# Performance work log

Measured on AMD Instinct MI355X. Metric: run time of the kernel, lower is better.

Reference implementation:

```python
import jax, jax.numpy as jnp
import numpy as np

B, N, K = 8, 2048, 20
IN_CHAN = 3
CONV_DIMS = (64, 64, 128, 256)
FEAT_DIM = 1024
SLOPE = 0.2  # LeakyReLU negative slope (DGCNN standard)


def setup_inputs() -> dict:
    key = jax.random.key(0)
    ks = jax.random.split(key, 11)
    x = jax.random.normal(ks[0], (B, N, IN_CHAN), dtype=jnp.float32)
    in_dims = (IN_CHAN,) + CONV_DIMS[:-1]
    inp = {"x": x}
    for i, (cin, cout) in enumerate(zip(in_dims, CONV_DIMS)):
        inp[f"W{i+1}"] = jax.random.normal(ks[1 + 2 * i], (cout, 2 * cin), dtype=jnp.float32) * 0.05
        inp[f"b{i+1}"] = jnp.zeros((cout,), dtype=jnp.float32)
    inp["Wf"] = jax.random.normal(ks[9], (FEAT_DIM, sum(CONV_DIMS)), dtype=jnp.float32) * 0.05
    inp["bf"] = jnp.zeros((FEAT_DIM,), dtype=jnp.float32)
    return inp


def _knn_idx(x, k):
    # x: (B, N, C) -> indices of k nearest neighbors (self included), (B, N, K)
    xx = jnp.sum(x * x, axis=-1)                       # (B, N)
    inner = jnp.einsum('bnc,bmc->bnm', x, x)           # (B, N, N)
    d2 = xx[:, :, None] - 2.0 * inner + xx[:, None, :]  # squared distances
    _, idx = jax.lax.top_k(-d2, k)                     # k smallest distances
    return idx


def _edge_conv(x, W, b, k):
    # x: (B, N, C); W: (O, 2C); b: (O,) -> (B, N, O)
    idx = _knn_idx(x, k)                               # (B, N, K)
    nbr = jax.vmap(lambda xb, ib: xb[ib])(x, idx)      # (B, N, K, C) gather
    center = jnp.broadcast_to(x[:, :, None, :], nbr.shape)
    feat = jnp.concatenate([nbr - center, center], axis=-1)  # (B, N, K, 2C)
    h = jnp.einsum('bnkc,oc->bnko', feat, W) + b       # 1x1 conv over edges
    h = jax.nn.leaky_relu(h, SLOPE)
    return jnp.max(h, axis=2)                          # max over neighbors


def reference(x, W1, b1, W2, b2, W3, b3, W4, b4, Wf, bf):
    params = [(W1, b1), (W2, b2), (W3, b3), (W4, b4)]
    feats = []
    h = x
    for W, b in params:
        h = _edge_conv(h, W, b, K)
        feats.append(h)
    hcat = jnp.concatenate(feats, axis=-1)             # (B, N, sum(conv_dims))
    out = jnp.einsum('bnc,oc->bno', hcat, Wf) + bf     # final 1x1 conv
    out = jax.nn.leaky_relu(out, SLOPE)
    return jnp.max(out, axis=1)                        # global max pool -> (B, FEAT_DIM)
```

## Files before the change

### kernel.cpp

```cpp
#include <hip/hip_runtime.h>

constexpr int B_ = 8;
constexpr int N_ = 2048;
constexpr int K_ = 20;
constexpr float SLOPE_ = 0.2f;

typedef __attribute__((ext_vector_type(8))) short bf16x8;
typedef __attribute__((ext_vector_type(8))) _Float16 f16x8;
typedef __attribute__((ext_vector_type(4))) float f32x4;

__device__ __forceinline__ float lrelu(float v) { return v > 0.0f ? v : SLOPE_ * v; }

__device__ __forceinline__ void async16(const void* g, void* l) {
  __builtin_amdgcn_global_load_lds((const __attribute__((address_space(1))) unsigned int*)g,
                                   (__attribute__((address_space(3))) unsigned int*)l, 16, 0, 0);
}

__device__ __forceinline__ unsigned long long shflx64(unsigned long long v, int m) {
  return __shfl_xor(v, m, 64);
}

__device__ __forceinline__ unsigned short f2bf(float f) {
  unsigned u = __float_as_uint(f);
  u += 0x7fff + ((u >> 16) & 1);
  return (unsigned short)(u >> 16);
}

__device__ __forceinline__ unsigned short f2h(float f) {
  _Float16 h = (_Float16)f;
  return __builtin_bit_cast(unsigned short, h);
}
__device__ __forceinline__ float h2f(unsigned short u) {
  return (float)__builtin_bit_cast(_Float16, u);
}

__global__ void prep_wp(const float* __restrict__ W, float* __restrict__ Wp, int O, int C) {
  int i = blockIdx.x * 256 + threadIdx.x;
  if (i >= 2 * O * C) return;
  int o = i / C, c = i - o * C;
  if (o < O)
    Wp[i] = W[o * 2 * C + c];
  else
    Wp[i] = W[(o - O) * 2 * C + C + c] - W[(o - O) * 2 * C + c];
}

__global__ void cvt_bf16(const float4* __restrict__ src, ushort4* __restrict__ dst, int n4) {
  int i = blockIdx.x * 256 + threadIdx.x;
  if (i >= n4) return;
  float4 v = src[i];
  ushort4 o = {f2bf(v.x), f2bf(v.y), f2bf(v.z), f2bf(v.w)};
  dst[i] = o;
}

__global__ void norms_x(const float* __restrict__ x, float* __restrict__ xx) {
  int i = blockIdx.x * 256 + threadIdx.x;
  if (i >= B_ * N_) return;
  const float* p = x + (size_t)i * 3;
  xx[i] = p[0] * p[0] + p[1] * p[1] + p[2] * p[2];
}

__global__ void split32_x(const float* __restrict__ x, unsigned short* __restrict__ xh,
                          unsigned short* __restrict__ xm) {
  int id = blockIdx.x * 256 + threadIdx.x;
  if (id >= B_ * N_ * 32) return;
  int row = id >> 5, c = id & 31;
  float val = (c < 3) ? x[row * 3 + c] : 0.0f;
  unsigned short hb = f2h(val);
  float vh = h2f(hb);
  xh[id] = hb;
  xm[id] = f2h(val - vh);
}

template <int C>
__global__ void pack_knn(const unsigned short* __restrict__ Xh,
                         const unsigned short* __restrict__ Xm,
                         unsigned short* __restrict__ Pk) {
  constexpr int KK = C / 32;
  int id = blockIdx.x * 256 + threadIdx.x;
  const int outoff = id;
  const int l = id & 63;
  id >>= 6;
  const int split = id & 1;
  id >>= 1;
  const int kk = id % KK;
  id /= KK;
  const int tile = id & 127;
  const int b = id >> 7;
  const unsigned short* src = (split == 0) ? Xh : Xm;
  const size_t soff =
      (size_t)(b * N_ + tile * 16 + (l & 15)) * C + (size_t)kk * 32 + (size_t)(l >> 4) * 8;
  uint4 v = *(const uint4*)(src + soff);
  *(uint4*)(Pk + (size_t)outoff * 8) = v;
}

template <int C>
__global__ __launch_bounds__(1024, 4) void knn_mfma(const unsigned short* __restrict__ Pk,
                                                    const unsigned short* __restrict__ Xh,
                                                    const unsigned short* __restrict__ Xm,
                                                    const float* __restrict__ xx,
                                                    int* __restrict__ idxo) {
  constexpr int KK = C / 32;
  constexpr int DP = 3;
  constexpr int NIT = KK * 8;
  const int b = blockIdx.x & 7;
  const int q0 = (blockIdx.x >> 3) * 16;
  const int tid = threadIdx.x;
  const int w = tid >> 6, lane = tid & 63;
  const int bN = b * N_;
  const int lr = lane & 15;
  const int lk = (lane >> 4) * 8;

  __shared__ float d2s[16][2052];
  __shared__ unsigned long long cbuf[16][64];

  const size_t qoff = (size_t)(bN + q0 + lr) * C + lk;
  f16x8 a2h[2], a2m[2];
  a2h[0] = *(const f16x8*)(Xh + qoff);
  a2m[0] = *(const f16x8*)(Xm + qoff);

  f32x4 acc[8];
#pragma unroll
  for (int t = 0; t < 8; t++) acc[t] = (f32x4){0.0f, 0.0f, 0.0f, 0.0f};

  const size_t pbase = (size_t)b * (128 * KK * 2 * 512) + (size_t)lane * 8;
  f16x8 bh[DP], bm[DP];
#pragma unroll
  for (int i = 0; i < DP; i++) {
    const size_t a = pbase + (size_t)(((w * 8 + i) * KK + 0) * 2) * 512;
    bh[i] = *(const f16x8*)(Pk + a);
    bm[i] = *(const f16x8*)(Pk + a + 512);
  }
#pragma unroll
  for (int it = 0; it < NIT; it++) {
    const int kk = it >> 3, t = it & 7, s = it % DP;
    if (t == 0 && kk + 1 < KK) {
      const size_t qa = qoff + (size_t)(kk + 1) * 32;
      a2h[(kk + 1) & 1] = *(const f16x8*)(Xh + qa);
      a2m[(kk + 1) & 1] = *(const f16x8*)(Xm + qa);
    }
    f16x8 vh = bh[s], vm = bm[s];
    if (it + DP < NIT) {
      const int it2 = it + DP;
      const int kk2 = it2 >> 3, t2 = it2 & 7;
      const size_t a = pbase + (size_t)(((w * 8 + t2) * KK + kk2) * 2) * 512;
      bh[s] = *(const f16x8*)(Pk + a);
      bm[s] = *(const f16x8*)(Pk + a + 512);
    }
    const f16x8 ah = a2h[kk & 1], am = a2m[kk & 1];
    acc[t] = __builtin_amdgcn_mfma_f32_16x16x32_f16(ah, vh, acc[t], 0, 0, 0);
    acc[t] = __builtin_amdgcn_mfma_f32_16x16x32_f16(ah, vm, acc[t], 0, 0, 0);
    acc[t] = __builtin_amdgcn_mfma_f32_16x16x32_f16(am, vh, acc[t], 0, 0, 0);
    acc[t] = __builtin_amdgcn_mfma_f32_16x16x32_f16(am, vm, acc[t], 0, 0, 0);
  }

  float qn[4];
#pragma unroll
  for (int r = 0; r < 4; r++) qn[r] = xx[bN + q0 + (lane >> 4) * 4 + r];
#pragma unroll
  for (int t = 0; t < 8; t++) {
    float cn = xx[bN + (w * 8 + t) * 16 + lr];
#pragma unroll
    for (int r = 0; r < 4; r++) {
      float v = fmaxf(fmaf(-2.0f, acc[t][r], cn + qn[r]), 0.0f);
      d2s[(lane >> 4) * 4 + r][(w * 8 + t) * 16 + lr] = v;
    }
  }
  __syncthreads();

  float r2[32];
#pragma unroll
  for (int i = 0; i < 32; i++) r2[i] = d2s[w][i * 64 + lane];

  const float INF = __int_as_float(0x7f800000);
  unsigned long long* cb = cbuf[w];
  int* outp = idxo + (size_t)(bN + q0 + w) * K_;

  float lmin = r2[0];
#pragma unroll
  for (int i = 1; i < 32; i++) lmin = fminf(lmin, r2[i]);
  float sv = lmin;
#pragma unroll
  for (int k = 2; k <= 64; k <<= 1)
#pragma unroll
    for (int j = k >> 1; j > 0; j >>= 1) {
      float p = __shfl_xor(sv, j, 64);
      bool takeMax = ((lane & j) != 0) == ((lane & k) == 0);
      sv = takeMax ? fmaxf(sv, p) : fminf(sv, p);
    }
  float T = __shfl(sv, 19, 64);

  unsigned cnt = 0;
#pragma unroll
  for (int i = 0; i < 32; i++) {
    bool pred = r2[i] <= T;
    unsigned long long mk = __ballot(pred);
    if (mk) {
      int off = __popcll(mk & ((1ull << lane) - 1ull));
      unsigned pos = cnt + (unsigned)off;
      if (pred && pos < 64)
        cb[pos] = ((unsigned long long)__float_as_uint(r2[i]) << 32) | (unsigned)(i * 64 + lane);
      cnt += (unsigned)__popcll(mk);
    }
  }

  if (cnt <= 64) {
    unsigned long long v = (lane < (int)cnt) ? cb[lane] : ~0ull;
#pragma unroll
    for (int k = 2; k <= 64; k <<= 1)
#pragma unroll
      for (int j = k >> 1; j > 0; j >>= 1) {
        unsigned long long p = shflx64(v, j);
        bool takeMax = ((lane & j) != 0) == ((lane & k) == 0);
        bool lt = v < p;
        v = (takeMax == lt) ? p : v;
      }
    if (lane < K_) outp[lane] = (int)(unsigned)(v & 0xffffffffull);
  } else {
    for (int t2 = 0; t2 < K_; t2++) {
      unsigned long long loc = ~0ull;
#pragma unroll
      for (int i = 0; i < 32; i++) {
        unsigned long long u =
            ((unsigned long long)__float_as_uint(r2[i]) << 32) | (unsigned)(i * 64 + lane);
        loc = u < loc ? u : loc;
      }
#pragma unroll
      for (int off = 32; off > 0; off >>= 1) {
        unsigned long long vv = shflx64(loc, off);
        loc = vv < loc ? vv : loc;
      }
      const int mwin = (int)(unsigned)(loc & 0xffffffffull);
      if (lane == 0) outp[t2] = mwin;
#pragma unroll
      for (int i = 0; i < 32; i++)
        if (i * 64 + lane == mwin) r2[i] = INF;
    }
  }
}

template <int C, int O2>
__global__ void proj_kernel(const float* __restrict__ hin, int stride,
                            const float* __restrict__ Wp, float* __restrict__ P) {
  const int nt = (blockIdx.x & 7) * N_ + (blockIdx.x >> 3) * 16;
  const int o = blockIdx.y * blockDim.x + threadIdx.x;
  __shared__ float hs[16][C];
  for (int i = threadIdx.x; i < 16 * C; i += blockDim.x) {
    int r = i / C, c = i - r * C;
    hs[r][c] = hin[(size_t)(nt + r) * stride + c];
  }
  __syncthreads();
  float acc[16];
#pragma unroll
  for (int t = 0; t < 16; t++) acc[t] = 0.0f;
  const float* wr = Wp + (size_t)o * C;
  if constexpr (C % 4 == 0) {
    for (int cg = 0; cg < C; cg += 4) {
      float4 w = *(const float4*)(wr + cg);
#pragma unroll
      for (int t = 0; t < 16; t++) {
        float4 h = *(const float4*)(&hs[t][cg]);
        acc[t] += w.x * h.x + w.y * h.y + w.z * h.z + w.w * h.w;
      }
    }
  } else {
    for (int c = 0; c < C; c++) {
      float w = wr[c];
#pragma unroll
      for (int t = 0; t < 16; t++) acc[t] += w * hs[t][c];
    }
  }
#pragma unroll
  for (int t = 0; t < 16; t++) P[(size_t)(nt + t) * O2 + o] = acc[t];
}

__global__ __launch_bounds__(256) void gemm_proj(const unsigned short* __restrict__ A, int astride,
                                                 const unsigned short* __restrict__ Bw,
                                                 float* __restrict__ P) {
  const int m0 = ((blockIdx.x & 7) * 16 + (blockIdx.x >> 3)) * 128;
  const int n0 = blockIdx.y * 128;
  const int tid = threadIdx.x;
  const int w = tid >> 6, lane = tid & 63;
  const int wm = w & 1, wn = w >> 1;

  __shared__ unsigned short lA[128 * 32];
  __shared__ unsigned short lB[128 * 32];

  const int r0 = (w * 2 + 0) * 16 + (lane >> 2);
  const int r1 = (w * 2 + 1) * 16 + (lane >> 2);
  const int ks = (lane & 3) * 8;
  const unsigned short* a0 = A + (size_t)(m0 + r0) * astride + ks;
  const unsigned short* a1 = A + (size_t)(m0 + r1) * astride + ks;
  const unsigned short* b0 = Bw + (size_t)(n0 + r0) * 128 + ks;
  const unsigned short* b1 = Bw + (size_t)(n0 + r1) * 128 + ks;
  unsigned short* lA0 = lA + (w * 2 + 0) * 512;
  unsigned short* lA1 = lA + (w * 2 + 1) * 512;
  unsigned short* lB0 = lB + (w * 2 + 0) * 512;
  unsigned short* lB1 = lB + (w * 2 + 1) * 512;

  f32x4 acc[4][4] = {};
  const int ka = (lane >> 4) * 8;

  for (int k0 = 0; k0 < 128; k0 += 32) {
    __syncthreads();
    async16(a0 + k0, lA0);
    async16(a1 + k0, lA1);
    async16(b0 + k0, lB0);
    async16(b1 + k0, lB1);
    __syncthreads();
    bf16x8 af[4], bfr[4];
#pragma unroll
    for (int mt = 0; mt < 4; mt++)
      af[mt] = *(const bf16x8*)&lA[(wm * 64 + mt * 16 + (lane & 15)) * 32 + ka];
#pragma unroll
    for (int nt = 0; nt < 4; nt++)
      bfr[nt] = *(const bf16x8*)&lB[(wn * 64 + nt * 16 + (lane & 15)) * 32 + ka];
#pragma unroll
    for (int mt = 0; mt < 4; mt++)
#pragma unroll
      for (int nt = 0; nt < 4; nt++)
        acc[mt][nt] = __builtin_amdgcn_mfma_f32_16x16x32_bf16(af[mt], bfr[nt], acc[mt][nt], 0, 0, 0);
  }

  const int col = n0 + wn * 64 + (lane & 15);
  const int rowb = m0 + wm * 64 + (lane >> 4) * 4;
#pragma unroll
  for (int mt = 0; mt < 4; mt++)
#pragma unroll
    for (int nt = 0; nt < 4; nt++)
#pragma unroll
      for (int r = 0; r < 4; r++)
        P[(size_t)(rowb + mt * 16 + r) * 512 + col + nt * 16] = acc[mt][nt][r];
}

template <int O>
__global__ __launch_bounds__(256) void combine_kernel(
    const float* __restrict__ P, const int* __restrict__ idxo, const float* __restrict__ bias,
    float* __restrict__ hout, float* __restrict__ xxo, unsigned short* __restrict__ xh,
    unsigned short* __restrict__ xm, unsigned short* __restrict__ a4) {
  constexpr int ROWS = 256 / O;
  const int bb = blockIdx.x & 7;
  const int rt = blockIdx.x >> 3;
  const int r = threadIdx.x / O;
  const int o = threadIdx.x & (O - 1);
  const int row = bb * N_ + rt * ROWS + r;
  __shared__ int idxs[ROWS][K_];
  __shared__ float ps[ROWS][O / 64 > 0 ? O / 64 : 1];
  if (o < K_) idxs[r][o] = idxo[(size_t)row * K_ + o];
  __syncthreads();
  const int base_row = bb * N_;
  float g = -3.4e38f;
#pragma unroll
  for (int k = 0; k < K_; k++) {
    float v = P[(size_t)(base_row + idxs[r][k]) * (2 * O) + o];
    g = fmaxf(g, v);
  }
  float ba = P[(size_t)row * (2 * O) + O + o];
  float val = lrelu(g + ba + bias[o]);
  hout[(size_t)row * 512 + o] = val;
  if (xh) {
    unsigned short hb = f2h(val);
    float vh = h2f(hb);
    size_t pp = (size_t)row * O + o;
    xh[pp] = hb;
    xm[pp] = f2h(val - vh);
  }
  if (a4) a4[(size_t)row * 1024 + o] = f2bf(val);
  if (xxo) {
    float sq = val * val;
#pragma unroll
    for (int off = 32; off > 0; off >>= 1) sq += __shfl_xor(sq, off, 64);
    if constexpr (O == 64) {
      if (o == 0) xxo[row] = sq;
    } else {
      if ((threadIdx.x & 63) == 0) ps[r][o >> 6] = sq;
      __syncthreads();
      if (o == 0) {
        float t = ps[r][0];
#pragma unroll
        for (int u = 1; u < O / 64; u++) t += ps[r][u];
        xxo[row] = t;
      }
    }
  }
}

__global__ __launch_bounds__(256) void gemm_final(const unsigned short* __restrict__ A,
                                                  const unsigned short* __restrict__ Bw,
                                                  float* __restrict__ part) {
  const int mt5 = (blockIdx.x & 7) * 16 + (blockIdx.x >> 3);
  const int m0 = mt5 * 128;
  const int n0 = blockIdx.y * 128;
  const int tid = threadIdx.x;
  const int w = tid >> 6, lane = tid & 63;
  const int wm = w & 1, wn = w >> 1;

  __shared__ unsigned short lA[128 * 32];
  __shared__ unsigned short lB[128 * 32];
  __shared__ float ldsred[2][128];

  const int r0 = (w * 2 + 0) * 16 + (lane >> 2);
  const int r1 = (w * 2 + 1) * 16 + (lane >> 2);
  const int ks = (lane & 3) * 8;
  const unsigned short* a0 = A + (size_t)(m0 + r0) * 512 + ks;
  const unsigned short* a1 = A + (size_t)(m0 + r1) * 512 + ks;
  const unsigned short* b0 = Bw + (size_t)(n0 + r0) * 512 + ks;
  const unsigned short* b1 = Bw + (size_t)(n0 + r1) * 512 + ks;
  unsigned short* lA0 = lA + (w * 2 + 0) * 512;
  unsigned short* lA1 = lA + (w * 2 + 1) * 512;
  unsigned short* lB0 = lB + (w * 2 + 0) * 512;
  unsigned short* lB1 = lB + (w * 2 + 1) * 512;

  f32x4 acc[4][4] = {};
  const int ka = (lane >> 4) * 8;

  for (int k0 = 0; k0 < 512; k0 += 32) {
    __syncthreads();
    async16(a0 + k0, lA0);
    async16(a1 + k0, lA1);
    async16(b0 + k0, lB0);
    async16(b1 + k0, lB1);
    __syncthreads();
    bf16x8 af[4], bfr[4];
#pragma unroll
    for (int mt = 0; mt < 4; mt++)
      af[mt] = *(const bf16x8*)&lA[(wm * 64 + mt * 16 + (lane & 15)) * 32 + ka];
#pragma unroll
    for (int nt = 0; nt < 4; nt++)
      bfr[nt] = *(const bf16x8*)&lB[(wn * 64 + nt * 16 + (lane & 15)) * 32 + ka];
#pragma unroll
    for (int mt = 0; mt < 4; mt++)
#pragma unroll
      for (int nt = 0; nt < 4; nt++)
        acc[mt][nt] = __builtin_amdgcn_mfma_f32_16x16x32_bf16(af[mt], bfr[nt], acc[mt][nt], 0, 0, 0);
  }

#pragma unroll
  for (int nt = 0; nt < 4; nt++) {
    float v = -3.4e38f;
#pragma unroll
    for (int mt = 0; mt < 4; mt++)
#pragma unroll
      for (int r = 0; r < 4; r++) v = fmaxf(v, acc[mt][nt][r]);
    v = fmaxf(v, __shfl_xor(v, 16, 64));
    v = fmaxf(v, __shfl_xor(v, 32, 64));
    if (lane < 16) ldsred[wm][wn * 64 + nt * 16 + lane] = v;
  }
  __syncthreads();
  if (tid < 128) {
    float v = fmaxf(ldsred[0][tid], ldsred[1][tid]);
    const int b = blockIdx.x & 7, s5 = blockIdx.x >> 3;
    part[(size_t)(b * 16 + s5) * 1024 + n0 + tid] = v;
  }
}

__global__ void final_reduce(const float* __restrict__ part, const float* __restrict__ bf,
                             float* __restrict__ out) {
  int i = blockIdx.x * 256 + threadIdx.x;
  if (i >= B_ * 1024) return;
  int b = i >> 10, o = i & 1023;
  float m = -3.4e38f;
  for (int s = 0; s < 16; s++) m = fmaxf(m, part[(size_t)(b * 16 + s) * 1024 + o]);
  out[i] = lrelu(m + bf[o]);
}

extern "C" void kernel_launch(void* const* d_in, const int* in_sizes, int n_in, void* d_out,
                              int out_size, void* d_ws, size_t ws_size, hipStream_t stream) {
  (void)in_sizes; (void)n_in; (void)out_size; (void)ws_size;
  const float* x = (const float*)d_in[0];
  const float* W1 = (const float*)d_in[1];
  const float* b1 = (const float*)d_in[2];
  const float* W2 = (const float*)d_in[3];
  const float* b2 = (const float*)d_in[4];
  const float* W3 = (const float*)d_in[5];
  const float* b3 = (const float*)d_in[6];
  const float* W4 = (const float*)d_in[7];
  const float* b4 = (const float*)d_in[8];
  const float* Wf = (const float*)d_in[9];
  const float* bf = (const float*)d_in[10];

  float* ws = (float*)d_ws;
  float* hcat = ws;
  float* P = hcat + (size_t)B_ * N_ * 512;
  int* idx = (int*)(P + (size_t)B_ * N_ * 512);
  float* Wp = (float*)(idx + (size_t)B_ * N_ * K_);
  float* part = Wp + 512 * 128;
  float* xxb = part + 8 * 16 * 1024;
  float* out = (float*)d_out;
  unsigned short* hcat_bf = (unsigned short*)P;
  unsigned short* Wf_bf = hcat_bf + (size_t)B_ * N_ * 512;
  unsigned short* A4_bf = (unsigned short*)hcat + 512;
  unsigned short* Wp_bf = (unsigned short*)part;

  unsigned short* Xh23 = (unsigned short*)(P + (size_t)2097152);
  unsigned short* Xm23 = Xh23 + (size_t)B_ * N_ * 64;
  unsigned short* Xh4 = (unsigned short*)(P + (size_t)4194304);
  unsigned short* Xm4 = Xh4 + (size_t)B_ * N_ * 128;
  unsigned short* Xh1 = Xh23;
  unsigned short* Xm1 = Xh1 + (size_t)B_ * N_ * 32;
  unsigned short* Pk = (unsigned short*)P;

  dim3 knng16(N_ / 16 * B_);
  const int pk_blocks32 = B_ * 128 * 1 * 2 * 64 / 256;
  const int pk_blocks64 = B_ * 128 * 2 * 2 * 64 / 256;
  const int pk_blocks128 = B_ * 128 * 4 * 2 * 64 / 256;

  prep_wp<<<(2 * 64 * 3 + 255) / 256, 256, 0, stream>>>(W1, Wp, 64, 3);
  norms_x<<<(B_ * N_ + 255) / 256, 256, 0, stream>>>(x, xxb);
  split32_x<<<(B_ * N_ * 32 + 255) / 256, 256, 0, stream>>>(x, Xh1, Xm1);
  pack_knn<32><<<pk_blocks32, 256, 0, stream>>>(Xh1, Xm1, Pk);
  knn_mfma<32><<<knng16, 1024, 0, stream>>>(Pk, Xh1, Xm1, xxb, idx);
  proj_kernel<3, 128><<<dim3(B_ * N_ / 16, 1), 128, 0, stream>>>(x, 3, Wp, P);
  combine_kernel<64><<<B_ * N_ / 4, 256, 0, stream>>>(P, idx, b1, hcat + 0, xxb, Xh23, Xm23,
                                                      nullptr);

  prep_wp<<<(2 * 64 * 64 + 255) / 256, 256, 0, stream>>>(W2, Wp, 64, 64);
  pack_knn<64><<<pk_blocks64, 256, 0, stream>>>(Xh23, Xm23, Pk);
  knn_mfma<64><<<knng16, 1024, 0, stream>>>(Pk, Xh23, Xm23, xxb, idx);
  proj_kernel<64, 128><<<dim3(B_ * N_ / 16, 1), 128, 0, stream>>>(hcat + 0, 512, Wp, P);
  combine_kernel<64><<<B_ * N_ / 4, 256, 0, stream>>>(P, idx, b2, hcat + 64, xxb, Xh23, Xm23,
                                                      nullptr);

  prep_wp<<<(2 * 128 * 64 + 255) / 256, 256, 0, stream>>>(W3, Wp, 128, 64);
  pack_knn<64><<<pk_blocks64, 256, 0, stream>>>(Xh23, Xm23, Pk);
  knn_mfma<64><<<knng16, 1024, 0, stream>>>(Pk, Xh23, Xm23, xxb, idx);
  proj_kernel<64, 256><<<dim3(B_ * N_ / 16, 1), 256, 0, stream>>>(hcat + 64, 512, Wp, P);
  combine_kernel<128><<<B_ * N_ / 2, 256, 0, stream>>>(P, idx, b3, hcat + 128, xxb, Xh4, Xm4,
                                                       A4_bf);

  prep_wp<<<(2 * 256 * 128 + 255) / 256, 256, 0, stream>>>(W4, Wp, 256, 128);
  pack_knn<128><<<pk_blocks128, 256, 0, stream>>>(Xh4, Xm4, Pk);
  knn_mfma<128><<<knng16, 1024, 0, stream>>>(Pk, Xh4, Xm4, xxb, idx);
  cvt_bf16<<<(512 * 128 / 4 + 255) / 256, 256, 0, stream>>>(
      (const float4*)Wp, (ushort4*)Wp_bf, 512 * 128 / 4);
  gemm_proj<<<dim3(B_ * N_ / 128, 4), 256, 0, stream>>>(A4_bf, 1024, Wp_bf, P);
  combine_kernel<256><<<B_ * N_, 256, 0, stream>>>(P, idx, b4, hcat + 256, nullptr, nullptr,
                                                   nullptr, nullptr);

  cvt_bf16<<<(B_ * N_ * 512 / 4 + 255) / 256, 256, 0, stream>>>(
      (const float4*)hcat, (ushort4*)hcat_bf, B_ * N_ * 512 / 4);
  cvt_bf16<<<(1024 * 512 / 4 + 255) / 256, 256, 0, stream>>>(
      (const float4*)Wf, (ushort4*)Wf_bf, 1024 * 512 / 4);
  gemm_final<<<dim3(128, 8), 256, 0, stream>>>(hcat_bf, Wf_bf, part);
  final_reduce<<<(B_ * 1024 + 255) / 256, 256, 0, stream>>>(part, bf, out);
}
```

Before: 461.6 us.

## Process 32 queries per KNN block to halve candidate-tile reloads

Each KNN block now handles 32 query points instead of 16. Pairs of waves share a candidate slice, so each wave computes 16 candidate tiles for one 16-query group. Distances are written to shared memory and top-k selection runs in two phases that reuse the 16-row buffer, which halves the number of blocks and the global loads of packed candidate data. The cost is twice as many accumulator registers, an extra syncthreads per K-chunk, serialized selection phases, and a simpler prefetch pipeline that may expose load latency.

```diff
diff --git a/kernel.cpp b/kernel.cpp
--- a/kernel.cpp
+++ b/kernel.cpp
@@ -93,87 +93,14 @@
   *(uint4*)(Pk + (size_t)outoff * 8) = v;
 }
 
-template <int C>
-__global__ __launch_bounds__(1024, 4) void knn_mfma(const unsigned short* __restrict__ Pk,
-                                                    const unsigned short* __restrict__ Xh,
-                                                    const unsigned short* __restrict__ Xm,
-                                                    const float* __restrict__ xx,
-                                                    int* __restrict__ idxo) {
-  constexpr int KK = C / 32;
-  constexpr int DP = 3;
-  constexpr int NIT = KK * 8;
-  const int b = blockIdx.x & 7;
-  const int q0 = (blockIdx.x >> 3) * 16;
-  const int tid = threadIdx.x;
-  const int w = tid >> 6, lane = tid & 63;
-  const int bN = b * N_;
-  const int lr = lane & 15;
-  const int lk = (lane >> 4) * 8;
-
-  __shared__ float d2s[16][2052];
-  __shared__ unsigned long long cbuf[16][64];
-
-  const size_t qoff = (size_t)(bN + q0 + lr) * C + lk;
-  f16x8 a2h[2], a2m[2];
-  a2h[0] = *(const f16x8*)(Xh + qoff);
-  a2m[0] = *(const f16x8*)(Xm + qoff);
-
-  f32x4 acc[8];
-#pragma unroll
-  for (int t = 0; t < 8; t++) acc[t] = (f32x4){0.0f, 0.0f, 0.0f, 0.0f};
-
-  const size_t pbase = (size_t)b * (128 * KK * 2 * 512) + (size_t)lane * 8;
-  f16x8 bh[DP], bm[DP];
-#pragma unroll
-  for (int i = 0; i < DP; i++) {
-    const size_t a = pbase + (size_t)(((w * 8 + i) * KK + 0) * 2) * 512;
-    bh[i] = *(const f16x8*)(Pk + a);
-    bm[i] = *(const f16x8*)(Pk + a + 512);
-  }
-#pragma unroll
-  for (int it = 0; it < NIT; it++) {
-    const int kk = it >> 3, t = it & 7, s = it % DP;
-    if (t == 0 && kk + 1 < KK) {
-      const size_t qa = qoff + (size_t)(kk + 1) * 32;
-      a2h[(kk + 1) & 1] = *(const f16x8*)(Xh + qa);
-      a2m[(kk + 1) & 1] = *(const f16x8*)(Xm + qa);
-    }
-    f16x8 vh = bh[s], vm = bm[s];
-    if (it + DP < NIT) {
-      const int it2 = it + DP;
-      const int kk2 = it2 >> 3, t2 = it2 & 7;
-      const size_t a = pbase + (size_t)(((w * 8 + t2) * KK + kk2) * 2) * 512;
-      bh[s] = *(const f16x8*)(Pk + a);
-      bm[s] = *(const f16x8*)(Pk + a + 512);
-    }
-    const f16x8 ah = a2h[kk & 1], am = a2m[kk & 1];
-    acc[t] = __builtin_amdgcn_mfma_f32_16x16x32_f16(ah, vh, acc[t], 0, 0, 0);
-    acc[t] = __builtin_amdgcn_mfma_f32_16x16x32_f16(ah, vm, acc[t], 0, 0, 0);
-    acc[t] = __builtin_amdgcn_mfma_f32_16x16x32_f16(am, vh, acc[t], 0, 0, 0);
-    acc[t] = __builtin_amdgcn_mfma_f32_16x16x32_f16(am, vm, acc[t], 0, 0, 0);
-  }
-
-  float qn[4];
-#pragma unroll
-  for (int r = 0; r < 4; r++) qn[r] = xx[bN + q0 + (lane >> 4) * 4 + r];
-#pragma unroll
-  for (int t = 0; t < 8; t++) {
-    float cn = xx[bN + (w * 8 + t) * 16 + lr];
-#pragma unroll
-    for (int r = 0; r < 4; r++) {
-      float v = fmaxf(fmaf(-2.0f, acc[t][r], cn + qn[r]), 0.0f);
-      d2s[(lane >> 4) * 4 + r][(w * 8 + t) * 16 + lr] = v;
-    }
-  }
-  __syncthreads();
-
+__device__ __forceinline__ void select_topk(const float* __restrict__ d2row, int lane,
+                                            unsigned long long* __restrict__ cb,
+                                            int* __restrict__ outp) {
   float r2[32];
 #pragma unroll
-  for (int i = 0; i < 32; i++) r2[i] = d2s[w][i * 64 + lane];
+  for (int i = 0; i < 32; i++) r2[i] = d2row[i * 64 + lane];
 
   const float INF = __int_as_float(0x7f800000);
-  unsigned long long* cb = cbuf[w];
-  int* outp = idxo + (size_t)(bN + q0 + w) * K_;
 
   float lmin = r2[0];
 #pragma unroll
@@ -235,6 +162,82 @@
       for (int i = 0; i < 32; i++)
         if (i * 64 + lane == mwin) r2[i] = INF;
     }
+  }
+}
+
+template <int C>
+__global__ __launch_bounds__(1024, 4) void knn_mfma(const unsigned short* __restrict__ Pk,
+                                                    const unsigned short* __restrict__ Xh,
+                                                    const unsigned short* __restrict__ Xm,
+                                                    const float* __restrict__ xx,
+                                                    int* __restrict__ idxo) {
+  constexpr int KK = C / 32;
+  const int b = blockIdx.x & 7;
+  const int q0 = (blockIdx.x >> 3) * 32;
+  const int tid = threadIdx.x;
+  const int w = tid >> 6, lane = tid & 63;
+  const int qg = w & 1, ws = w >> 1;
+  const int bN = b * N_;
+  const int lr = lane & 15;
+  const int lk = (lane >> 4) * 8;
+
+  __shared__ float d2s[16][2052];
+  __shared__ unsigned long long cbuf[16][64];
+
+  const size_t qoff = (size_t)(bN + q0 + qg * 16 + lr) * C + lk;
+
+  f32x4 acc[16];
+#pragma unroll
+  for (int t = 0; t < 16; t++) acc[t] = (f32x4){0.0f, 0.0f, 0.0f, 0.0f};
+
+  const size_t pbase = (size_t)b * (128 * KK * 2 * 512) + (size_t)lane * 8;
+  for (int kk = 0; kk < KK; kk++) {
+    if (kk > 0) __syncthreads();
+    const f16x8 ah = *(const f16x8*)(Xh + qoff + (size_t)kk * 32);
+    const f16x8 am = *(const f16x8*)(Xm + qoff + (size_t)kk * 32);
+    f16x8 bh[2], bm[2];
+#pragma unroll
+    for (int i = 0; i < 2; i++) {
+      const size_t a = pbase + (size_t)(((ws * 16 + i) * KK + kk) * 2) * 512;
+      bh[i] = *(const f16x8*)(Pk + a);
+      bm[i] = *(const f16x8*)(Pk + a + 512);
+    }
+#pragma unroll
+    for (int t = 0; t < 16; t++) {
+      const int s = t & 1;
+      f16x8 vh = bh[s], vm = bm[s];
+      if (t + 2 < 16) {
+        const size_t a = pbase + (size_t)(((ws * 16 + t + 2) * KK + kk) * 2) * 512;
+        bh[s] = *(const f16x8*)(Pk + a);
+        bm[s] = *(const f16x8*)(Pk + a + 512);
+      }
+      acc[t] = __builtin_amdgcn_mfma_f32_16x16x32_f16(ah, vh, acc[t], 0, 0, 0);
+      acc[t] = __builtin_amdgcn_mfma_f32_16x16x32_f16(ah, vm, acc[t], 0, 0, 0);
+      acc[t] = __builtin_amdgcn_mfma_f32_16x16x32_f16(am, vh, acc[t], 0, 0, 0);
+      acc[t] = __builtin_amdgcn_mfma_f32_16x16x32_f16(am, vm, acc[t], 0, 0, 0);
+    }
+  }
+
+  float qn[4];
+#pragma unroll
+  for (int r = 0; r < 4; r++) qn[r] = xx[bN + q0 + qg * 16 + (lane >> 4) * 4 + r];
+
+#pragma unroll
+  for (int ph = 0; ph < 2; ph++) {
+    if (qg == ph) {
+#pragma unroll
+      for (int t = 0; t < 16; t++) {
+        const int tt = ws * 16 + t;
+        float cn = xx[bN + tt * 16 + lr];
+#pragma unroll
+        for (int r = 0; r < 4; r++)
+          d2s[(lane >> 4) * 4 + r][tt * 16 + lr] =
+              fmaxf(fmaf(-2.0f, acc[t][r], cn + qn[r]), 0.0f);
+      }
+    }
+    __syncthreads();
+    select_topk(&d2s[w][0], lane, cbuf[w], idxo + (size_t)(bN + q0 + ph * 16 + w) * K_);
+    if (ph == 0) __syncthreads();
   }
 }
 
@@ -499,7 +502,7 @@
   unsigned short* Xm1 = Xh1 + (size_t)B_ * N_ * 32;
   unsigned short* Pk = (unsigned short*)P;
 
-  dim3 knng16(N_ / 16 * B_);
+  dim3 knng32q(N_ / 32 * B_);
   const int pk_blocks32 = B_ * 128 * 1 * 2 * 64 / 256;
   const int pk_blocks64 = B_ * 128 * 2 * 2 * 64 / 256;
   const int pk_blocks128 = B_ * 128 * 4 * 2 * 64 / 256;
@@ -508,28 +511,28 @@
   norms_x<<<(B_ * N_ + 255) / 256, 256, 0, stream>>>(x, xxb);
   split32_x<<<(B_ * N_ * 32 + 255) / 256, 256, 0, stream>>>(x, Xh1, Xm1);
   pack_knn<32><<<pk_blocks32, 256, 0, stream>>>(Xh1, Xm1, Pk);
-  knn_mfma<32><<<knng16, 1024, 0, stream>>>(Pk, Xh1, Xm1, xxb, idx);
+  knn_mfma<32><<<knng32q, 1024, 0, stream>>>(Pk, Xh1, Xm1, xxb, idx);
   proj_kernel<3, 128><<<dim3(B_ * N_ / 16, 1), 128, 0, stream>>>(x, 3, Wp, P);
   combine_kernel<64><<<B_ * N_ / 4, 256, 0, stream>>>(P, idx, b1, hcat + 0, xxb, Xh23, Xm23,
                                                       nullptr);
 
   prep_wp<<<(2 * 64 * 64 + 255) / 256, 256, 0, stream>>>(W2, Wp, 64, 64);
   pack_knn<64><<<pk_blocks64, 256, 0, stream>>>(Xh23, Xm23, Pk);
-  knn_mfma<64><<<knng16, 1024, 0, stream>>>(Pk, Xh23, Xm23, xxb, idx);
+  knn_mfma<64><<<knng32q, 1024, 0, stream>>>(Pk, Xh23, Xm23, xxb, idx);
   proj_kernel<64, 128><<<dim3(B_ * N_ / 16, 1), 128, 0, stream>>>(hcat + 0, 512, Wp, P);
   combine_kernel<64><<<B_ * N_ / 4, 256, 0, stream>>>(P, idx, b2, hcat + 64, xxb, Xh23, Xm23,
                                                       nullptr);
 
   prep_wp<<<(2 * 128 * 64 + 255) / 256, 256, 0, stream>>>(W3, Wp, 128, 64);
   pack_knn<64><<<pk_blocks64, 256, 0, stream>>>(Xh23, Xm23, Pk);
-  knn_mfma<64><<<knng16, 1024, 0, stream>>>(Pk, Xh23, Xm23, xxb, idx);
+  knn_mfma<64><<<knng32q, 1024, 0, stream>>>(Pk, Xh23, Xm23, xxb, idx);
   proj_kernel<64, 256><<<dim3(B_ * N_ / 16, 1), 256, 0, stream>>>(hcat + 64, 512, Wp, P);
   combine_kernel<128><<<B_ * N_ / 2, 256, 0, stream>>>(P, idx, b3, hcat + 128, xxb, Xh4, Xm4,
                                                        A4_bf);
 
   prep_wp<<<(2 * 256 * 128 + 255) / 256, 256, 0, stream>>>(W4, Wp, 256, 128);
   pack_knn<128><<<pk_blocks128, 256, 0, stream>>>(Xh4, Xm4, Pk);
-  knn_mfma<128><<<knng16, 1024, 0, stream>>>(Pk, Xh4, Xm4, xxb, idx);
+  knn_mfma<128><<<knng32q, 1024, 0, stream>>>(Pk, Xh4, Xm4, xxb, idx);
   cvt_bf16<<<(512 * 128 / 4 + 255) / 256, 256, 0, stream>>>(
       (const float4*)Wp, (ushort4*)Wp_bf, 512 * 128 / 4);
   gemm_proj<<<dim3(B_ * N_ / 128, 4), 256, 0, stream>>>(A4_bf, 1024, Wp_bf, P);
```

After: 550.3 us. 19.2% more time.
